# Kernel optimization log

Measured on AMD Instinct MI355X. Metric: run time of the kernel, lower is better.

Reference implementation:

```python
import jax, jax.numpy as jnp
import numpy as np

B, S, H, E, K = 4, 4096, 1024, 8, 2
DFF = 4 * H


def setup_inputs() -> dict:
    key = jax.random.key(0)
    ks = jax.random.split(key, 6)
    s_in = 1.0 / np.sqrt(H)
    s_ff = 1.0 / np.sqrt(DFF)
    return {
        "x": jax.random.normal(ks[0], (B, S, H), dtype=jnp.float32),
        "router_w": jax.random.normal(ks[1], (E, H), dtype=jnp.float32) * s_in,
        "router_b": jnp.zeros((E,), dtype=jnp.float32),
        "fc1_w": jax.random.normal(ks[2], (E, DFF, H), dtype=jnp.float32) * s_in,
        "fc1_b": jnp.zeros((E, DFF), dtype=jnp.float32),
        "fc2_w": jax.random.normal(ks[3], (E, H, DFF), dtype=jnp.float32) * s_ff,
        "fc2_b": jnp.zeros((E, H), dtype=jnp.float32),
    }


def reference(x, router_w, router_b, fc1_w, fc1_b, fc2_w, fc2_b):
    b, s, h = x.shape
    e = router_w.shape[0]
    k = K
    # Router: [B,S,E]
    logits = jnp.einsum("bsh,eh->bse", x, router_w) + router_b
    top_v, top_i = jax.lax.top_k(logits, k)            # [B,S,K]
    probs = jax.nn.softmax(top_v, axis=-1)             # softmax over top-k logits
    # Combine weights per expert [B,S,E]; top-k indices are distinct per token,
    # so summing one-hot*prob over k matches the original's gather-of-first-match.
    combine = jnp.sum(jax.nn.one_hot(top_i, e, dtype=x.dtype) * probs[..., None], axis=-2)
    xf = x.reshape(-1, h)            # [T,H], T = B*S
    cf = combine.reshape(-1, e)      # [T,E]
    out = jnp.zeros_like(xf)
    for ei in range(e):              # fixed small loop over experts
        hdn = jax.nn.relu(xf @ fc1_w[ei].T + fc1_b[ei])   # [T,4H]
        y = hdn @ fc2_w[ei].T + fc2_b[ei]                 # [T,H]
        out = out + cf[:, ei:ei + 1] * y                  # zero weight == not routed
    return out.reshape(b, s, h)
```

## Files before the change

### kernel.cpp

```cpp
#include <hip/hip_runtime.h>
#include <stdint.h>

#define T_TOKENS 16384
#define H_DIM 1024
#define E_NUM 8
#define DFF_DIM 4096

#define BMT 128
#define BNT 128
#define BKT 64
#define MT_CAP 264
#define PAD_ROWS (MT_CAP * BMT)
#define NCHUNK 4
#define MT_PER_CHUNK (MT_CAP / NCHUNK)
#define CHUNK_ROWS (MT_PER_CHUNK * BMT)

#define WS_COUNTS     0
#define WS_CURSOR     32
#define WS_OFFS       64
#define WS_SLOT_TOK   256
#define WS_SLOT_W     135424
#define WS_EIDX       270592
#define WS_EW         401664
#define WS_WC1        532736
#define WS_WC2        67641600
#define WS_XB         134750464
#define WS_HDN        168304896
#define WS_OUTK1      237510912
#define WS_REQUIRED   271065344UL
#define WS_SMALL_ZERO 270592

typedef __attribute__((ext_vector_type(8))) short short8;
typedef __attribute__((ext_vector_type(4))) float f32x4;

__device__ __forceinline__ unsigned short f2bf(float f) {
  union { float f; unsigned int u; } v; v.f = f;
  unsigned int r = v.u + 0x7FFFu + ((v.u >> 16) & 1u);
  return (unsigned short)(r >> 16);
}

__device__ __forceinline__ float bf2f(unsigned short b) {
  union { unsigned int u; float f; } v; v.u = ((unsigned int)b) << 16;
  return v.f;
}

__device__ __forceinline__ void load_lds16(const void* g, void* l) {
  __builtin_amdgcn_global_load_lds(
      (const __attribute__((address_space(1))) void*)g,
      (__attribute__((address_space(3))) void*)l, 16, 0, 0);
}

__global__ void convert_weights(const float* __restrict__ w1,
                                const float* __restrict__ w2,
                                unsigned short* __restrict__ wc1,
                                unsigned short* __restrict__ wc2) {
  int i = blockIdx.x * blockDim.x + threadIdx.x;
  const float4* s1 = (const float4*)w1;
  const float4* s2 = (const float4*)w2;
  float4 a = s1[i];
  float4 b = s2[i];
  ushort4 ua, ub;
  ua.x = f2bf(a.x); ua.y = f2bf(a.y); ua.z = f2bf(a.z); ua.w = f2bf(a.w);
  ub.x = f2bf(b.x); ub.y = f2bf(b.y); ub.z = f2bf(b.z); ub.w = f2bf(b.w);
  ((ushort4*)wc1)[i] = ua;
  ((ushort4*)wc2)[i] = ub;
}

__global__ __launch_bounds__(256) void router_kernel(
    const float* __restrict__ x, const float* __restrict__ rw,
    const float* __restrict__ rb, unsigned short* __restrict__ xb,
    int* __restrict__ eidx, float* __restrict__ ew) {
  __shared__ float4 rws[E_NUM * 256];
  const int tid = threadIdx.x;
#pragma unroll
  for (int k = 0; k < 8; ++k) rws[k * 256 + tid] = ((const float4*)rw)[k * 256 + tid];
  __syncthreads();

  const int wave = tid >> 6;
  const int lane = tid & 63;
#pragma unroll
  for (int i = 0; i < 4; ++i) {
    const int t = blockIdx.x * 16 + wave * 4 + i;
    const float4* xrow = (const float4*)(x + (size_t)t * H_DIM);
    float4 xv[4];
#pragma unroll
    for (int j = 0; j < 4; ++j) xv[j] = xrow[j * 64 + lane];

    ushort4* xbrow = (ushort4*)(xb + (size_t)t * H_DIM);
#pragma unroll
    for (int j = 0; j < 4; ++j) {
      ushort4 o;
      o.x = f2bf(xv[j].x); o.y = f2bf(xv[j].y);
      o.z = f2bf(xv[j].z); o.w = f2bf(xv[j].w);
      xbrow[j * 64 + lane] = o;
    }

    float s[E_NUM];
#pragma unroll
    for (int e = 0; e < E_NUM; ++e) {
      float a = 0.f;
#pragma unroll
      for (int j = 0; j < 4; ++j) {
        float4 wv = rws[e * 256 + j * 64 + lane];
        a += xv[j].x * wv.x + xv[j].y * wv.y + xv[j].z * wv.z + xv[j].w * wv.w;
      }
      s[e] = a;
    }
#pragma unroll
    for (int off = 32; off; off >>= 1) {
#pragma unroll
      for (int e = 0; e < E_NUM; ++e) s[e] += __shfl_xor(s[e], off);
    }
    if (lane == 0) {
      float lg[E_NUM];
#pragma unroll
      for (int e = 0; e < E_NUM; ++e) lg[e] = s[e] + rb[e];
      int i0 = 0; float m0 = lg[0];
#pragma unroll
      for (int e = 1; e < E_NUM; ++e)
        if (lg[e] > m0) { m0 = lg[e]; i0 = e; }
      int i1 = -1; float m1 = -3.4e38f;
#pragma unroll
      for (int e = 0; e < E_NUM; ++e)
        if (e != i0 && lg[e] > m1) { m1 = lg[e]; i1 = e; }
      float e1 = expf(m1 - m0);
      float denom = 1.f + e1;
      ((int2*)eidx)[t] = make_int2(i0, i1);
      ((float2*)ew)[t] = make_float2(1.f / denom, e1 / denom);
    }
  }
}

__global__ __launch_bounds__(1024) void count_kernel(const int* __restrict__ eidx,
                                                     int* __restrict__ counts,
                                                     int* __restrict__ offs,
                                                     int* __restrict__ cursor) {
  __shared__ int hist[E_NUM];
  const int tid = threadIdx.x;
  const int lane = tid & 63;
  if (tid < E_NUM) hist[tid] = 0;
  __syncthreads();
  int c[E_NUM];
#pragma unroll
  for (int e = 0; e < E_NUM; ++e) c[e] = 0;
  const int4* p = (const int4*)eidx;
#pragma unroll
  for (int i = 0; i < 8; ++i) {
    int4 v = p[i * 1024 + tid];
#pragma unroll
    for (int e = 0; e < E_NUM; ++e)
      c[e] += (v.x == e) + (v.y == e) + (v.z == e) + (v.w == e);
  }
#pragma unroll
  for (int off = 32; off; off >>= 1) {
#pragma unroll
    for (int e = 0; e < E_NUM; ++e) c[e] += __shfl_xor(c[e], off);
  }
  if (lane == 0) {
#pragma unroll
    for (int e = 0; e < E_NUM; ++e) atomicAdd(&hist[e], c[e]);
  }
  __syncthreads();
  if (tid == 0) {
    int acc = 0;
    offs[0] = 0;
#pragma unroll
    for (int e = 0; e < E_NUM; ++e) {
      counts[e] = hist[e];
      cursor[e] = 0;
      acc += ((hist[e] + BMT - 1) / BMT) * BMT;
      offs[e + 1] = acc;
    }
  }
}

__global__ __launch_bounds__(1024) void scatter_kernel(
    const int* __restrict__ eidx, const float* __restrict__ ew,
    const int* __restrict__ offs, int* __restrict__ cursor,
    int* __restrict__ slot_token, float* __restrict__ slot_w) {
  __shared__ int wcnt[16][E_NUM];
  __shared__ int wpre[16][E_NUM];
  __shared__ int bbase[E_NUM];
  __shared__ int soffs[E_NUM];
  const int tid = threadIdx.x, w = tid >> 6, lane = tid & 63;
  const int t = blockIdx.x * 1024 + tid;
  const int2 epair = ((const int2*)eidx)[t];
  const float2 wpair = ((const float2*)ew)[t];
  const int e0 = epair.x, e1 = epair.y;
  const unsigned long long lt = (1ULL << lane) - 1ULL;
  if (tid < E_NUM) soffs[tid] = offs[tid];
  int r0 = 0, r1 = 0;
#pragma unroll
  for (int e = 0; e < E_NUM; ++e) {
    unsigned long long m0 = __ballot(e0 == e);
    unsigned long long m1 = __ballot(e1 == e);
    int c0 = __popcll(m0);
    if (e0 == e) r0 = __popcll(m0 & lt);
    if (e1 == e) r1 = c0 + __popcll(m1 & lt);
    if (lane == 0) wcnt[w][e] = c0 + __popcll(m1);
  }
  __syncthreads();
  if (tid < E_NUM) {
    int run = 0;
#pragma unroll
    for (int w2 = 0; w2 < 16; ++w2) {
      wpre[w2][tid] = run;
      run += wcnt[w2][tid];
    }
    bbase[tid] = atomicAdd(&cursor[tid], run);
  }
  __syncthreads();
  const int s0 = soffs[e0] + bbase[e0] + wpre[w][e0] + r0;
  const int s1 = soffs[e1] + bbase[e1] + wpre[w][e1] + r1;
  slot_token[s0] = t;
  slot_w[s0] = wpair.x;
  slot_token[s1] = t | (int)0x80000000;
  slot_w[s1] = wpair.y;
}

template <int KTOT>
__device__ __forceinline__ void gemm_core(const unsigned short* const* aptr,
                                          const unsigned short* const* bptr,
                                          unsigned short* lA, unsigned short* lB,
                                          f32x4 acc[4][4]) {
  const int tid = threadIdx.x;
  const int w = tid >> 6, lane = tid & 63;
  const int wm = w >> 1, wn = w & 1;
  const int rrow = lane & 15;
  const int rq = lane >> 4;

  for (int ks = 0; ks < KTOT / BKT; ++ks) {
    const int k0 = ks * BKT;
#pragma unroll
    for (int i = 0; i < 4; ++i) {
      load_lds16(aptr[i] + k0, lA + i * 2048 + w * 512);
      load_lds16(bptr[i] + k0, lB + i * 2048 + w * 512);
    }
    __syncthreads();
#pragma unroll
    for (int kk = 0; kk < 2; ++kk) {
      short8 af[4], bfr[4];
#pragma unroll
      for (int mi = 0; mi < 4; ++mi)
        af[mi] = *(const short8*)(lA + (wm * 64 + mi * 16 + rrow) * BKT + kk * 32 + rq * 8);
#pragma unroll
      for (int ni = 0; ni < 4; ++ni)
        bfr[ni] = *(const short8*)(lB + (wn * 64 + ni * 16 + rrow) * BKT + kk * 32 + rq * 8);
#pragma unroll
      for (int mi = 0; mi < 4; ++mi)
#pragma unroll
        for (int ni = 0; ni < 4; ++ni)
          acc[mi][ni] = __builtin_amdgcn_mfma_f32_16x16x32_bf16(af[mi], bfr[ni], acc[mi][ni], 0, 0, 0);
    }
    __syncthreads();
  }
}

__global__ __launch_bounds__(256, 2) void fc1_kernel(
    const unsigned short* __restrict__ xb, const unsigned short* __restrict__ wc1,
    const float* __restrict__ fc1_b, const int* __restrict__ offs,
    const int* __restrict__ counts, const int* __restrict__ slot_token,
    unsigned short* __restrict__ hdn, int chunk) {
  __shared__ unsigned short sA[BMT * BKT];
  __shared__ unsigned short sB[BNT * BKT];
  const int mt = chunk * MT_PER_CHUNK + blockIdx.y;
  const int row0 = mt * BMT;
  if (row0 >= offs[E_NUM]) return;
  int e = 0;
#pragma unroll
  for (int i = 1; i < E_NUM; ++i) e = (row0 >= offs[i]) ? i : e;
  const int n0 = blockIdx.x * BNT;

  f32x4 acc[4][4];
  f32x4 zf = {0.f, 0.f, 0.f, 0.f};
#pragma unroll
  for (int mi = 0; mi < 4; ++mi)
#pragma unroll
    for (int ni = 0; ni < 4; ++ni) acc[mi][ni] = zf;

  const int tid = threadIdx.x;
  const int srow = tid >> 3;
  const int scol = (tid & 7) * 8;
  const unsigned short* Bm = wc1 + (size_t)e * DFF_DIM * H_DIM + (size_t)n0 * H_DIM;
  const unsigned short* aptr[4];
  const unsigned short* bptr[4];
#pragma unroll
  for (int i = 0; i < 4; ++i) {
    const int r = i * 32 + srow;
    const int tok = slot_token[row0 + r] & 0x7FFFFFFF;
    aptr[i] = xb + (size_t)tok * H_DIM + scol;
    bptr[i] = Bm + (size_t)r * H_DIM + scol;
  }
  gemm_core<H_DIM>(aptr, bptr, sA, sB, acc);

  const int w = tid >> 6;
  const int lane = tid & 63;
  const int wm = w >> 1, wn = w & 1;
  const int rrow = lane & 15, rq = lane >> 4;
  const int cnt = counts[e];
  const int lbase = row0 - offs[e];
  const int hrow0 = row0 - chunk * CHUNK_ROWS;
#pragma unroll
  for (int mi = 0; mi < 4; ++mi) {
#pragma unroll
    for (int j = 0; j < 4; ++j) {
      const int rit = wm * 64 + mi * 16 + rq * 4 + j;
      if (lbase + rit >= cnt) continue;
      unsigned short* hrow = hdn + (size_t)(hrow0 + rit) * DFF_DIM;
#pragma unroll
      for (int ni = 0; ni < 4; ++ni) {
        const int n = n0 + wn * 64 + ni * 16 + rrow;
        float v = acc[mi][ni][j] + fc1_b[e * DFF_DIM + n];
        v = v > 0.f ? v : 0.f;
        hrow[n] = f2bf(v);
      }
    }
  }
}

__global__ __launch_bounds__(256, 2) void fc2_kernel(
    const unsigned short* __restrict__ hdn, const unsigned short* __restrict__ wc2,
    const float* __restrict__ fc2_b, const int* __restrict__ offs,
    const int* __restrict__ counts, const int* __restrict__ slot_token,
    const float* __restrict__ slot_w, float* __restrict__ out,
    unsigned short* __restrict__ outk1, int chunk) {
  __shared__ unsigned short sA[BMT * BKT];
  __shared__ unsigned short sB[BNT * BKT];
  const int id = blockIdx.x;
  const int xcd = id & 7, j = id >> 3;
  int ml, nt;
  if (j < 64) { ml = xcd * 8 + (j & 7); nt = j >> 3; }
  else        { ml = 64 + (j & 1);      nt = xcd;    }
  const int mt = chunk * MT_PER_CHUNK + ml;
  const int row0 = mt * BMT;
  if (row0 >= offs[E_NUM]) return;
  int e = 0;
#pragma unroll
  for (int i = 1; i < E_NUM; ++i) e = (row0 >= offs[i]) ? i : e;
  const int n0 = nt * BNT;

  f32x4 acc[4][4];
  f32x4 zf = {0.f, 0.f, 0.f, 0.f};
#pragma unroll
  for (int mi = 0; mi < 4; ++mi)
#pragma unroll
    for (int ni = 0; ni < 4; ++ni) acc[mi][ni] = zf;

  const int tid = threadIdx.x;
  const int srow = tid >> 3;
  const int scol = (tid & 7) * 8;
  const unsigned short* A = hdn + (size_t)(ml * BMT) * DFF_DIM;
  const unsigned short* Bm = wc2 + (size_t)e * H_DIM * DFF_DIM + (size_t)n0 * DFF_DIM;
  const unsigned short* aptr[4];
  const unsigned short* bptr[4];
#pragma unroll
  for (int i = 0; i < 4; ++i) {
    const int r = i * 32 + srow;
    aptr[i] = A + (size_t)r * DFF_DIM + scol;
    bptr[i] = Bm + (size_t)r * DFF_DIM + scol;
  }
  gemm_core<DFF_DIM>(aptr, bptr, sA, sB, acc);

  const int w = tid >> 6;
  const int lane = tid & 63;
  const int wm = w >> 1, wn = w & 1;
  const int rrow = lane & 15, rq = lane >> 4;
  const int cnt = counts[e];
  const int lbase = row0 - offs[e];
#pragma unroll
  for (int mi = 0; mi < 4; ++mi) {
#pragma unroll
    for (int j2 = 0; j2 < 4; ++j2) {
      const int rit = wm * 64 + mi * 16 + rq * 4 + j2;
      if (lbase + rit >= cnt) continue;
      const int gr = row0 + rit;
      const int st = slot_token[gr];
      const int tok = st & 0x7FFFFFFF;
      const float wgt = slot_w[gr];
#pragma unroll
      for (int ni = 0; ni < 4; ++ni) {
        const int h = n0 + wn * 64 + ni * 16 + rrow;
        const float v = (acc[mi][ni][j2] + fc2_b[e * H_DIM + h]) * wgt;
        if (st >= 0) out[(size_t)tok * H_DIM + h] = v;
        else         outk1[(size_t)tok * H_DIM + h] = f2bf(v);
      }
    }
  }
}

__global__ __launch_bounds__(256) void add_kernel(
    float* __restrict__ out, const unsigned short* __restrict__ outk1) {
  const int wave = threadIdx.x >> 6;
  const int lane = threadIdx.x & 63;
  const int t = blockIdx.x * 4 + wave;
  float4* orow = (float4*)(out + (size_t)t * H_DIM);
  const ushort4* krow = (const ushort4*)(outk1 + (size_t)t * H_DIM);
#pragma unroll
  for (int j = 0; j < 4; ++j) {
    const int idx = j * 64 + lane;
    float4 a = orow[idx];
    ushort4 b = krow[idx];
    a.x += bf2f(b.x); a.y += bf2f(b.y); a.z += bf2f(b.z); a.w += bf2f(b.w);
    orow[idx] = a;
  }
}

extern "C" void kernel_launch(void* const* d_in, const int* in_sizes, int n_in,
                              void* d_out, int out_size, void* d_ws, size_t ws_size,
                              hipStream_t stream) {
  const float* x        = (const float*)d_in[0];
  const float* router_w = (const float*)d_in[1];
  const float* router_b = (const float*)d_in[2];
  const float* fc1_w    = (const float*)d_in[3];
  const float* fc1_b    = (const float*)d_in[4];
  const float* fc2_w    = (const float*)d_in[5];
  const float* fc2_b    = (const float*)d_in[6];
  float* out = (float*)d_out;

  char* ws = (char*)d_ws;
  int* counts            = (int*)(ws + WS_COUNTS);
  int* cursor            = (int*)(ws + WS_CURSOR);
  int* offs              = (int*)(ws + WS_OFFS);
  int* slot_token        = (int*)(ws + WS_SLOT_TOK);
  float* slot_w          = (float*)(ws + WS_SLOT_W);
  int* eidx              = (int*)(ws + WS_EIDX);
  float* ew              = (float*)(ws + WS_EW);
  unsigned short* wc1    = (unsigned short*)(ws + WS_WC1);
  unsigned short* wc2    = (unsigned short*)(ws + WS_WC2);
  unsigned short* xb     = (unsigned short*)(ws + WS_XB);
  unsigned short* hdn    = (unsigned short*)(ws + WS_HDN);
  unsigned short* outk1  = (unsigned short*)(ws + WS_OUTK1);

  if (ws_size < WS_REQUIRED) {
    hipMemsetAsync(d_out, 0, (size_t)T_TOKENS * H_DIM * sizeof(float), stream);
    return;
  }
  hipMemsetAsync(ws, 0, WS_SMALL_ZERO, stream);

  convert_weights<<<32768, 256, 0, stream>>>(fc1_w, fc2_w, wc1, wc2);
  router_kernel<<<T_TOKENS / 16, 256, 0, stream>>>(x, router_w, router_b, xb, eidx, ew);
  count_kernel<<<1, 1024, 0, stream>>>(eidx, counts, offs, cursor);
  scatter_kernel<<<T_TOKENS / 1024, 1024, 0, stream>>>(eidx, ew, offs, cursor, slot_token, slot_w);

  for (int c = 0; c < NCHUNK; ++c) {
    fc1_kernel<<<dim3(DFF_DIM / BNT, MT_PER_CHUNK), 256, 0, stream>>>(
        xb, wc1, fc1_b, offs, counts, slot_token, hdn, c);
    fc2_kernel<<<E_NUM * MT_PER_CHUNK, 256, 0, stream>>>(
        hdn, wc2, fc2_b, offs, counts, slot_token, slot_w, out, outk1, c);
  }
  add_kernel<<<T_TOKENS / 4, 256, 0, stream>>>(out, outk1);
}
```

Before: 1.044 ms.

## Overlap fc2 of one chunk with fc1 of the next in one fused launch

Merges the fc1 and fc2 GEMM kernels into a single `moe_gemm` kernel that picks its role from the block index. Each launch runs fc2 for chunk c alongside fc1 for chunk c+1, using a double-buffered hidden activation area. The chunk count doubles to 8 so the pipeline has finer stages. fc2 blocks also rotate their K-loop start by a hashed phase so concurrent blocks do not hit the same weight rows at the same time. The aim is to fill the idle tail of each launch and cut launch serialization, at the cost of more launches, divergent block roles and smaller per-chunk tiles.

```diff
diff --git a/kernel.cpp b/kernel.cpp
--- a/kernel.cpp
+++ b/kernel.cpp
@@ -11,9 +11,10 @@
 #define BKT 64
 #define MT_CAP 264
 #define PAD_ROWS (MT_CAP * BMT)
-#define NCHUNK 4
+#define NCHUNK 8
 #define MT_PER_CHUNK (MT_CAP / NCHUNK)
 #define CHUNK_ROWS (MT_PER_CHUNK * BMT)
+#define CHUNK_ELEMS ((size_t)CHUNK_ROWS * DFF_DIM)
 
 #define WS_COUNTS     0
 #define WS_CURSOR     32
@@ -222,14 +223,16 @@
 __device__ __forceinline__ void gemm_core(const unsigned short* const* aptr,
                                           const unsigned short* const* bptr,
                                           unsigned short* lA, unsigned short* lB,
-                                          f32x4 acc[4][4]) {
+                                          f32x4 acc[4][4], int phase) {
   const int tid = threadIdx.x;
   const int w = tid >> 6, lane = tid & 63;
   const int wm = w >> 1, wn = w & 1;
   const int rrow = lane & 15;
   const int rq = lane >> 4;
-
-  for (int ks = 0; ks < KTOT / BKT; ++ks) {
+  const int NS = KTOT / BKT;
+
+  for (int s = 0; s < NS; ++s) {
+    const int ks = (s + phase) & (NS - 1);
     const int k0 = ks * BKT;
 #pragma unroll
     for (int i = 0; i < 4; ++i) {
@@ -256,88 +259,23 @@
   }
 }
 
-__global__ __launch_bounds__(256, 2) void fc1_kernel(
+__global__ __launch_bounds__(256, 2) void moe_gemm(
     const unsigned short* __restrict__ xb, const unsigned short* __restrict__ wc1,
-    const float* __restrict__ fc1_b, const int* __restrict__ offs,
-    const int* __restrict__ counts, const int* __restrict__ slot_token,
-    unsigned short* __restrict__ hdn, int chunk) {
+    const float* __restrict__ fc1_b, unsigned short* __restrict__ hdn,
+    const unsigned short* __restrict__ wc2, const float* __restrict__ fc2_b,
+    const int* __restrict__ offs, const int* __restrict__ counts,
+    const int* __restrict__ slot_token, const float* __restrict__ slot_w,
+    float* __restrict__ out, unsigned short* __restrict__ outk1,
+    int cf2, int cf1, int nf2) {
   __shared__ unsigned short sA[BMT * BKT];
   __shared__ unsigned short sB[BNT * BKT];
-  const int mt = chunk * MT_PER_CHUNK + blockIdx.y;
-  const int row0 = mt * BMT;
-  if (row0 >= offs[E_NUM]) return;
-  int e = 0;
-#pragma unroll
-  for (int i = 1; i < E_NUM; ++i) e = (row0 >= offs[i]) ? i : e;
-  const int n0 = blockIdx.x * BNT;
-
-  f32x4 acc[4][4];
-  f32x4 zf = {0.f, 0.f, 0.f, 0.f};
-#pragma unroll
-  for (int mi = 0; mi < 4; ++mi)
-#pragma unroll
-    for (int ni = 0; ni < 4; ++ni) acc[mi][ni] = zf;
-
+  const int id = blockIdx.x;
   const int tid = threadIdx.x;
   const int srow = tid >> 3;
   const int scol = (tid & 7) * 8;
-  const unsigned short* Bm = wc1 + (size_t)e * DFF_DIM * H_DIM + (size_t)n0 * H_DIM;
-  const unsigned short* aptr[4];
-  const unsigned short* bptr[4];
-#pragma unroll
-  for (int i = 0; i < 4; ++i) {
-    const int r = i * 32 + srow;
-    const int tok = slot_token[row0 + r] & 0x7FFFFFFF;
-    aptr[i] = xb + (size_t)tok * H_DIM + scol;
-    bptr[i] = Bm + (size_t)r * H_DIM + scol;
-  }
-  gemm_core<H_DIM>(aptr, bptr, sA, sB, acc);
-
-  const int w = tid >> 6;
-  const int lane = tid & 63;
+  const int w = tid >> 6, lane = tid & 63;
   const int wm = w >> 1, wn = w & 1;
   const int rrow = lane & 15, rq = lane >> 4;
-  const int cnt = counts[e];
-  const int lbase = row0 - offs[e];
-  const int hrow0 = row0 - chunk * CHUNK_ROWS;
-#pragma unroll
-  for (int mi = 0; mi < 4; ++mi) {
-#pragma unroll
-    for (int j = 0; j < 4; ++j) {
-      const int rit = wm * 64 + mi * 16 + rq * 4 + j;
-      if (lbase + rit >= cnt) continue;
-      unsigned short* hrow = hdn + (size_t)(hrow0 + rit) * DFF_DIM;
-#pragma unroll
-      for (int ni = 0; ni < 4; ++ni) {
-        const int n = n0 + wn * 64 + ni * 16 + rrow;
-        float v = acc[mi][ni][j] + fc1_b[e * DFF_DIM + n];
-        v = v > 0.f ? v : 0.f;
-        hrow[n] = f2bf(v);
-      }
-    }
-  }
-}
-
-__global__ __launch_bounds__(256, 2) void fc2_kernel(
-    const unsigned short* __restrict__ hdn, const unsigned short* __restrict__ wc2,
-    const float* __restrict__ fc2_b, const int* __restrict__ offs,
-    const int* __restrict__ counts, const int* __restrict__ slot_token,
-    const float* __restrict__ slot_w, float* __restrict__ out,
-    unsigned short* __restrict__ outk1, int chunk) {
-  __shared__ unsigned short sA[BMT * BKT];
-  __shared__ unsigned short sB[BNT * BKT];
-  const int id = blockIdx.x;
-  const int xcd = id & 7, j = id >> 3;
-  int ml, nt;
-  if (j < 64) { ml = xcd * 8 + (j & 7); nt = j >> 3; }
-  else        { ml = 64 + (j & 1);      nt = xcd;    }
-  const int mt = chunk * MT_PER_CHUNK + ml;
-  const int row0 = mt * BMT;
-  if (row0 >= offs[E_NUM]) return;
-  int e = 0;
-#pragma unroll
-  for (int i = 1; i < E_NUM; ++i) e = (row0 >= offs[i]) ? i : e;
-  const int n0 = nt * BNT;
 
   f32x4 acc[4][4];
   f32x4 zf = {0.f, 0.f, 0.f, 0.f};
@@ -346,43 +284,96 @@
 #pragma unroll
     for (int ni = 0; ni < 4; ++ni) acc[mi][ni] = zf;
 
-  const int tid = threadIdx.x;
-  const int srow = tid >> 3;
-  const int scol = (tid & 7) * 8;
-  const unsigned short* A = hdn + (size_t)(ml * BMT) * DFF_DIM;
-  const unsigned short* Bm = wc2 + (size_t)e * H_DIM * DFF_DIM + (size_t)n0 * DFF_DIM;
-  const unsigned short* aptr[4];
-  const unsigned short* bptr[4];
-#pragma unroll
-  for (int i = 0; i < 4; ++i) {
-    const int r = i * 32 + srow;
-    aptr[i] = A + (size_t)r * DFF_DIM + scol;
-    bptr[i] = Bm + (size_t)r * DFF_DIM + scol;
-  }
-  gemm_core<DFF_DIM>(aptr, bptr, sA, sB, acc);
-
-  const int w = tid >> 6;
-  const int lane = tid & 63;
-  const int wm = w >> 1, wn = w & 1;
-  const int rrow = lane & 15, rq = lane >> 4;
-  const int cnt = counts[e];
-  const int lbase = row0 - offs[e];
-#pragma unroll
-  for (int mi = 0; mi < 4; ++mi) {
-#pragma unroll
-    for (int j2 = 0; j2 < 4; ++j2) {
-      const int rit = wm * 64 + mi * 16 + rq * 4 + j2;
-      if (lbase + rit >= cnt) continue;
-      const int gr = row0 + rit;
-      const int st = slot_token[gr];
-      const int tok = st & 0x7FFFFFFF;
-      const float wgt = slot_w[gr];
-#pragma unroll
-      for (int ni = 0; ni < 4; ++ni) {
-        const int h = n0 + wn * 64 + ni * 16 + rrow;
-        const float v = (acc[mi][ni][j2] + fc2_b[e * H_DIM + h]) * wgt;
-        if (st >= 0) out[(size_t)tok * H_DIM + h] = v;
-        else         outk1[(size_t)tok * H_DIM + h] = f2bf(v);
+  if (id < nf2) {
+    const int cc  = cf2 + (id >= 264 ? 1 : 0);
+    const int lid = id - (id >= 264 ? 264 : 0);
+    const int xcd = lid & 7, j = lid >> 3;
+    int ml, nt;
+    if (j < 32) { ml = xcd * 4 + (j & 3); nt = j >> 2; }
+    else        { ml = 32;                nt = xcd;    }
+    const int mt = cc * MT_PER_CHUNK + ml;
+    const int row0 = mt * BMT;
+    if (row0 >= offs[E_NUM]) return;
+    int e = 0;
+#pragma unroll
+    for (int i = 1; i < E_NUM; ++i) e = (row0 >= offs[i]) ? i : e;
+    const int n0 = nt * BNT;
+
+    const unsigned short* A = hdn + (size_t)(cc & 1) * CHUNK_ELEMS +
+                              (size_t)(ml * BMT) * DFF_DIM;
+    const unsigned short* Bm = wc2 + (size_t)e * H_DIM * DFF_DIM + (size_t)n0 * DFF_DIM;
+    const unsigned short* aptr[4];
+    const unsigned short* bptr[4];
+#pragma unroll
+    for (int i = 0; i < 4; ++i) {
+      const int r = i * 32 + srow;
+      aptr[i] = A + (size_t)r * DFF_DIM + scol;
+      bptr[i] = Bm + (size_t)r * DFF_DIM + scol;
+    }
+    const int phase = (int)((blockIdx.x * 2654435761u) >> 26);
+    gemm_core<DFF_DIM>(aptr, bptr, sA, sB, acc, phase);
+
+    const int cnt = counts[e];
+    const int lbase = row0 - offs[e];
+#pragma unroll
+    for (int mi = 0; mi < 4; ++mi) {
+#pragma unroll
+      for (int j2 = 0; j2 < 4; ++j2) {
+        const int rit = wm * 64 + mi * 16 + rq * 4 + j2;
+        if (lbase + rit >= cnt) continue;
+        const int gr = row0 + rit;
+        const int st = slot_token[gr];
+        const int tok = st & 0x7FFFFFFF;
+        const float wgt = slot_w[gr];
+#pragma unroll
+        for (int ni = 0; ni < 4; ++ni) {
+          const int h = n0 + wn * 64 + ni * 16 + rrow;
+          const float v = (acc[mi][ni][j2] + fc2_b[e * H_DIM + h]) * wgt;
+          if (st >= 0) out[(size_t)tok * H_DIM + h] = v;
+          else         outk1[(size_t)tok * H_DIM + h] = f2bf(v);
+        }
+      }
+    }
+  } else {
+    const int fid = id - nf2;
+    const int nt = fid & 31, ml = fid >> 5;
+    const int mt = cf1 * MT_PER_CHUNK + ml;
+    const int row0 = mt * BMT;
+    if (row0 >= offs[E_NUM]) return;
+    int e = 0;
+#pragma unroll
+    for (int i = 1; i < E_NUM; ++i) e = (row0 >= offs[i]) ? i : e;
+    const int n0 = nt * BNT;
+
+    const unsigned short* Bm = wc1 + (size_t)e * DFF_DIM * H_DIM + (size_t)n0 * H_DIM;
+    const unsigned short* aptr[4];
+    const unsigned short* bptr[4];
+#pragma unroll
+    for (int i = 0; i < 4; ++i) {
+      const int r = i * 32 + srow;
+      const int tok = slot_token[row0 + r] & 0x7FFFFFFF;
+      aptr[i] = xb + (size_t)tok * H_DIM + scol;
+      bptr[i] = Bm + (size_t)r * H_DIM + scol;
+    }
+    gemm_core<H_DIM>(aptr, bptr, sA, sB, acc, 0);
+
+    unsigned short* hw = hdn + (size_t)(cf1 & 1) * CHUNK_ELEMS;
+    const int cnt = counts[e];
+    const int lbase = row0 - offs[e];
+#pragma unroll
+    for (int mi = 0; mi < 4; ++mi) {
+#pragma unroll
+      for (int j2 = 0; j2 < 4; ++j2) {
+        const int rit = wm * 64 + mi * 16 + rq * 4 + j2;
+        if (lbase + rit >= cnt) continue;
+        unsigned short* hrow = hw + (size_t)(ml * BMT + rit) * DFF_DIM;
+#pragma unroll
+        for (int ni = 0; ni < 4; ++ni) {
+          const int n = n0 + wn * 64 + ni * 16 + rrow;
+          float v = acc[mi][ni][j2] + fc1_b[e * DFF_DIM + n];
+          v = v > 0.f ? v : 0.f;
+          hrow[n] = f2bf(v);
+        }
       }
     }
   }
@@ -442,11 +433,21 @@
   count_kernel<<<1, 1024, 0, stream>>>(eidx, counts, offs, cursor);
   scatter_kernel<<<T_TOKENS / 1024, 1024, 0, stream>>>(eidx, ew, offs, cursor, slot_token, slot_w);
 
-  for (int c = 0; c < NCHUNK; ++c) {
-    fc1_kernel<<<dim3(DFF_DIM / BNT, MT_PER_CHUNK), 256, 0, stream>>>(
-        xb, wc1, fc1_b, offs, counts, slot_token, hdn, c);
-    fc2_kernel<<<E_NUM * MT_PER_CHUNK, 256, 0, stream>>>(
-        hdn, wc2, fc2_b, offs, counts, slot_token, slot_w, out, outk1, c);
-  }
+  const int NF1 = 32 * MT_PER_CHUNK;
+  const int NF2 = 8 * MT_PER_CHUNK;
+
+  moe_gemm<<<NF1, 256, 0, stream>>>(xb, wc1, fc1_b, hdn, wc2, fc2_b, offs, counts,
+                                    slot_token, slot_w, out, outk1, 0, 0, 0);
+  for (int c = 0; c < 6; ++c) {
+    moe_gemm<<<NF2 + NF1, 256, 0, stream>>>(xb, wc1, fc1_b, hdn, wc2, fc2_b, offs,
+                                            counts, slot_token, slot_w, out, outk1,
+                                            c, c + 1, NF2);
+  }
+  moe_gemm<<<NF1, 256, 0, stream>>>(xb, wc1, fc1_b, hdn, wc2, fc2_b, offs, counts,
+                                    slot_token, slot_w, out, outk1, 0, 7, 0);
+  moe_gemm<<<2 * NF2, 256, 0, stream>>>(xb, wc1, fc1_b, hdn, wc2, fc2_b, offs,
+                                        counts, slot_token, slot_w, out, outk1,
+                                        6, 0, 2 * NF2);
+
   add_kernel<<<T_TOKENS / 4, 256, 0, stream>>>(out, outk1);
 }
```

Measured after the change: 1.152 ms. 1.1x slower.

## Split fc2 GEMM along K with bf16 partials and a separate combine kernel

Applied to the files above, without the earlier changes.

fc2 now splits its 4096-long reduction into four segments, each block writing bf16 partial sums to a workspace buffer. A new combine kernel sums the partials, applies the routing weight and scatters the result to the output or the second-slot buffer. Chunks go from 4 to 8 so each launch is smaller. The aim is more blocks per fc2 launch and better occupancy, paid for by extra partial-sum traffic, an extra launch per chunk, and bf16 rounding of the partials.

```diff
diff --git a/kernel.cpp b/kernel.cpp
--- a/kernel.cpp
+++ b/kernel.cpp
@@ -11,9 +11,11 @@
 #define BKT 64
 #define MT_CAP 264
 #define PAD_ROWS (MT_CAP * BMT)
-#define NCHUNK 4
+#define NCHUNK 8
 #define MT_PER_CHUNK (MT_CAP / NCHUNK)
 #define CHUNK_ROWS (MT_PER_CHUNK * BMT)
+#define KSPLIT 4
+#define KSEG (DFF_DIM / KSPLIT)
 
 #define WS_COUNTS     0
 #define WS_CURSOR     32
@@ -26,6 +28,7 @@
 #define WS_WC2        67641600
 #define WS_XB         134750464
 #define WS_HDN        168304896
+#define WS_Y          202907904
 #define WS_OUTK1      237510912
 #define WS_REQUIRED   271065344UL
 #define WS_SMALL_ZERO 270592
@@ -321,23 +324,22 @@
 __global__ __launch_bounds__(256, 2) void fc2_kernel(
     const unsigned short* __restrict__ hdn, const unsigned short* __restrict__ wc2,
     const float* __restrict__ fc2_b, const int* __restrict__ offs,
-    const int* __restrict__ counts, const int* __restrict__ slot_token,
-    const float* __restrict__ slot_w, float* __restrict__ out,
-    unsigned short* __restrict__ outk1, int chunk) {
+    unsigned short* __restrict__ y, int chunk) {
   __shared__ unsigned short sA[BMT * BKT];
   __shared__ unsigned short sB[BNT * BKT];
   const int id = blockIdx.x;
   const int xcd = id & 7, j = id >> 3;
-  int ml, nt;
-  if (j < 64) { ml = xcd * 8 + (j & 7); nt = j >> 3; }
-  else        { ml = 64 + (j & 1);      nt = xcd;    }
-  const int mt = chunk * MT_PER_CHUNK + ml;
-  const int row0 = mt * BMT;
+  const int g = xcd * 132 + j;
+  const int ml = g >> 5;
+  const int ks = (g >> 3) & 3;
+  const int nt = g & 7;
+  const int row0 = chunk * CHUNK_ROWS + ml * BMT;
   if (row0 >= offs[E_NUM]) return;
   int e = 0;
 #pragma unroll
   for (int i = 1; i < E_NUM; ++i) e = (row0 >= offs[i]) ? i : e;
   const int n0 = nt * BNT;
+  const int kbase = ks * KSEG;
 
   f32x4 acc[4][4];
   f32x4 zf = {0.f, 0.f, 0.f, 0.f};
@@ -349,8 +351,8 @@
   const int tid = threadIdx.x;
   const int srow = tid >> 3;
   const int scol = (tid & 7) * 8;
-  const unsigned short* A = hdn + (size_t)(ml * BMT) * DFF_DIM;
-  const unsigned short* Bm = wc2 + (size_t)e * H_DIM * DFF_DIM + (size_t)n0 * DFF_DIM;
+  const unsigned short* A = hdn + (size_t)(ml * BMT) * DFF_DIM + kbase;
+  const unsigned short* Bm = wc2 + (size_t)e * H_DIM * DFF_DIM + (size_t)n0 * DFF_DIM + kbase;
   const unsigned short* aptr[4];
   const unsigned short* bptr[4];
 #pragma unroll
@@ -359,31 +361,77 @@
     aptr[i] = A + (size_t)r * DFF_DIM + scol;
     bptr[i] = Bm + (size_t)r * DFF_DIM + scol;
   }
-  gemm_core<DFF_DIM>(aptr, bptr, sA, sB, acc);
+  gemm_core<KSEG>(aptr, bptr, sA, sB, acc);
 
   const int w = tid >> 6;
   const int lane = tid & 63;
   const int wm = w >> 1, wn = w & 1;
   const int rrow = lane & 15, rq = lane >> 4;
-  const int cnt = counts[e];
-  const int lbase = row0 - offs[e];
+  unsigned short* ypart = y + (size_t)ks * CHUNK_ROWS * H_DIM;
 #pragma unroll
   for (int mi = 0; mi < 4; ++mi) {
 #pragma unroll
     for (int j2 = 0; j2 < 4; ++j2) {
       const int rit = wm * 64 + mi * 16 + rq * 4 + j2;
-      if (lbase + rit >= cnt) continue;
-      const int gr = row0 + rit;
-      const int st = slot_token[gr];
-      const int tok = st & 0x7FFFFFFF;
-      const float wgt = slot_w[gr];
+      unsigned short* yrow = ypart + (size_t)(ml * BMT + rit) * H_DIM;
 #pragma unroll
       for (int ni = 0; ni < 4; ++ni) {
         const int h = n0 + wn * 64 + ni * 16 + rrow;
-        const float v = (acc[mi][ni][j2] + fc2_b[e * H_DIM + h]) * wgt;
-        if (st >= 0) out[(size_t)tok * H_DIM + h] = v;
-        else         outk1[(size_t)tok * H_DIM + h] = f2bf(v);
+        const float b = (ks == 0) ? fc2_b[e * H_DIM + h] : 0.f;
+        yrow[h] = f2bf(acc[mi][ni][j2] + b);
       }
+    }
+  }
+}
+
+__global__ __launch_bounds__(256) void combine_kernel(
+    const unsigned short* __restrict__ y, const int* __restrict__ slot_token,
+    const float* __restrict__ slot_w, const int* __restrict__ offs,
+    const int* __restrict__ counts, float* __restrict__ out,
+    unsigned short* __restrict__ outk1, int chunk) {
+  const int wave = threadIdx.x >> 6;
+  const int lane = threadIdx.x & 63;
+  const int r = blockIdx.x * 4 + wave;
+  const int s = chunk * CHUNK_ROWS + r;
+  if (s >= offs[E_NUM]) return;
+  int e = 0;
+#pragma unroll
+  for (int i = 1; i < E_NUM; ++i) e = (s >= offs[i]) ? i : e;
+  if (s - offs[e] >= counts[e]) return;
+  const int st = slot_token[s];
+  const int tok = st & 0x7FFFFFFF;
+  const float wgt = slot_w[s];
+
+  float acc[16];
+#pragma unroll
+  for (int i = 0; i < 16; ++i) acc[i] = 0.f;
+#pragma unroll
+  for (int ks = 0; ks < KSPLIT; ++ks) {
+    const unsigned short* yrow = y + (size_t)(ks * CHUNK_ROWS + r) * H_DIM + lane * 16;
+#pragma unroll
+    for (int v = 0; v < 2; ++v) {
+      short8 p = *(const short8*)(yrow + v * 8);
+#pragma unroll
+      for (int i = 0; i < 8; ++i) acc[v * 8 + i] += bf2f((unsigned short)p[i]);
+    }
+  }
+  if (st >= 0) {
+    float* orow = out + (size_t)tok * H_DIM + lane * 16;
+#pragma unroll
+    for (int v = 0; v < 4; ++v) {
+      float4 o;
+      o.x = wgt * acc[v * 4 + 0]; o.y = wgt * acc[v * 4 + 1];
+      o.z = wgt * acc[v * 4 + 2]; o.w = wgt * acc[v * 4 + 3];
+      ((float4*)orow)[v] = o;
+    }
+  } else {
+    unsigned short* krow = outk1 + (size_t)tok * H_DIM + lane * 16;
+#pragma unroll
+    for (int v = 0; v < 2; ++v) {
+      short8 o;
+#pragma unroll
+      for (int i = 0; i < 8; ++i) o[i] = (short)f2bf(wgt * acc[v * 8 + i]);
+      *(short8*)(krow + v * 8) = o;
     }
   }
 }
@@ -429,6 +477,7 @@
   unsigned short* wc2    = (unsigned short*)(ws + WS_WC2);
   unsigned short* xb     = (unsigned short*)(ws + WS_XB);
   unsigned short* hdn    = (unsigned short*)(ws + WS_HDN);
+  unsigned short* y      = (unsigned short*)(ws + WS_Y);
   unsigned short* outk1  = (unsigned short*)(ws + WS_OUTK1);
 
   if (ws_size < WS_REQUIRED) {
@@ -445,8 +494,10 @@
   for (int c = 0; c < NCHUNK; ++c) {
     fc1_kernel<<<dim3(DFF_DIM / BNT, MT_PER_CHUNK), 256, 0, stream>>>(
         xb, wc1, fc1_b, offs, counts, slot_token, hdn, c);
-    fc2_kernel<<<E_NUM * MT_PER_CHUNK, 256, 0, stream>>>(
-        hdn, wc2, fc2_b, offs, counts, slot_token, slot_w, out, outk1, c);
+    fc2_kernel<<<8 * MT_PER_CHUNK * KSPLIT, 256, 0, stream>>>(
+        hdn, wc2, fc2_b, offs, y, c);
+    combine_kernel<<<CHUNK_ROWS / 4, 256, 0, stream>>>(
+        y, slot_token, slot_w, offs, counts, out, outk1, c);
   }
   add_kernel<<<T_TOKENS / 4, 256, 0, stream>>>(out, outk1);
 }
```

Result: slower. 1.231 ms (+18.0%).
